# Performance work log

Hardware: AMD Instinct MI355X
Metric: run time of the kernel (lower is better)

The kernel has to match this reference:

```python
import jax, jax.numpy as jnp
import numpy as np
from jax import lax

TOP_K = 2
NHEAD = 8

def _ln(x, g, b, eps=1e-5):
    m = x.mean(-1, keepdims=True)
    v = x.var(-1, keepdims=True)
    return (x - m) / jnp.sqrt(v + eps) * g + b


def setup_inputs() -> dict:
    B, S, N = 32, 512, 32
    DT, D, E, HE, MO, LTX, LTCN, K = 64, 128, 16, 256, 128, 2, 4, 3
    keys = iter(jax.random.split(jax.random.key(0), 96))
    def rn(shape, s=0.05):
        return (jax.random.normal(next(keys), shape, jnp.float32) * s)
    inp = {}
    inp['x_features_globally_std'] = jax.random.normal(next(keys), (B, S, N), jnp.float32)
    counts = jax.random.randint(next(keys), (B,), 8, N + 1)
    inp['sensor_mask'] = (jnp.arange(N)[None, :] < counts[:, None]).astype(jnp.float32)
    inp['proj_w'] = rn((1, DT)); inp['proj_b'] = jnp.zeros(DT)
    inp['tcn_w1'] = rn((LTCN, DT, DT, K)); inp['tcn_b1'] = jnp.zeros((LTCN, DT))
    inp['tcn_w2'] = rn((LTCN, DT, DT, K)); inp['tcn_b2'] = jnp.zeros((LTCN, DT))
    inp['tcn_ln_g'] = jnp.ones(DT); inp['tcn_ln_b'] = jnp.zeros(DT)
    inp['pool_w'] = rn((DT, D)); inp['pool_b'] = jnp.zeros(D)
    inp['pos_inter'] = rn((1, N, D), 0.02)
    inp['tx_ln1_g'] = jnp.ones((LTX, D)); inp['tx_ln1_b'] = jnp.zeros((LTX, D))
    inp['tx_qkv_w'] = rn((LTX, D, 3 * D)); inp['tx_qkv_b'] = jnp.zeros((LTX, 3 * D))
    inp['tx_out_w'] = rn((LTX, D, D)); inp['tx_out_b'] = jnp.zeros((LTX, D))
    inp['tx_ln2_g'] = jnp.ones((LTX, D)); inp['tx_ln2_b'] = jnp.zeros((LTX, D))
    inp['tx_ff1_w'] = rn((LTX, D, 2 * D)); inp['tx_ff1_b'] = jnp.zeros((LTX, 2 * D))
    inp['tx_ff2_w'] = rn((LTX, 2 * D, D)); inp['tx_ff2_b'] = jnp.zeros((LTX, D))
    inp['tx_fln_g'] = jnp.ones(D); inp['tx_fln_b'] = jnp.zeros(D)
    inp['exp_w1'] = rn((E, D, HE)); inp['exp_b1'] = jnp.zeros((E, HE))
    inp['exp_w2'] = rn((E, HE, MO)); inp['exp_b2'] = jnp.zeros((E, MO))
    inp['gate_f_w'] = rn((2 * D, E)); inp['gate_f_b'] = jnp.zeros(E)
    inp['gate_fail_w'] = rn((2 * D, E)); inp['gate_fail_b'] = jnp.zeros(E)
    inp['gate_rca_w'] = rn((D, E)); inp['gate_rca_b'] = jnp.zeros(E)
    inp['pred_w'] = rn((DT + D + MO, 3)); inp['pred_b'] = jnp.zeros(3)
    inp['fail_w'] = rn((MO, 3)); inp['fail_b'] = jnp.zeros(3)
    inp['rca_w'] = rn((DT + D + MO, 1)); inp['rca_b'] = jnp.zeros(1)
    return inp


def reference(x_features_globally_std, sensor_mask, proj_w, proj_b, tcn_w1, tcn_b1, tcn_w2, tcn_b2,
              tcn_ln_g, tcn_ln_b, pool_w, pool_b, pos_inter, tx_ln1_g, tx_ln1_b, tx_qkv_w, tx_qkv_b,
              tx_out_w, tx_out_b, tx_ln2_g, tx_ln2_b, tx_ff1_w, tx_ff1_b, tx_ff2_w, tx_ff2_b,
              tx_fln_g, tx_fln_b, exp_w1, exp_b1, exp_w2, exp_b2, gate_f_w, gate_f_b,
              gate_fail_w, gate_fail_b, gate_rca_w, gate_rca_b, pred_w, pred_b, fail_w, fail_b, rca_w, rca_b):
    x = x_features_globally_std
    B, S, N = x.shape
    DT = proj_w.shape[1]; D = pool_w.shape[1]; E = gate_f_b.shape[0]
    K = tcn_w1.shape[-1]
    # per-sensor encoder: [B,S,N] -> [B*N, S, 1]
    x_enc = x.transpose(0, 2, 1).reshape(B * N, S, 1)
    h = x_enc @ proj_w + proj_b  # [BN,S,DT]
    # sinusoidal positional encoding
    pos = jnp.arange(S, dtype=jnp.float32)[:, None]
    div = jnp.exp(jnp.arange(0, DT, 2, dtype=jnp.float32) * (-np.log(10000.0) / DT))
    pe = jnp.zeros((S, DT), jnp.float32).at[:, 0::2].set(jnp.sin(pos * div)).at[:, 1::2].set(jnp.cos(pos * div))
    h = h + pe
    h = h.transpose(0, 2, 1)  # [BN, DT, S]
    for i in range(tcn_w1.shape[0]):
        dil = 2 ** i
        pad = (K - 1) * dil  # causal left pad == torch pad-both + trim right
        def conv(z, w, b):
            return lax.conv_general_dilated(z, w, (1,), [(pad, 0)], rhs_dilation=(dil,),
                                            dimension_numbers=('NCH', 'OIH', 'NCH')) + b[None, :, None]
        o = jax.nn.relu(conv(h, tcn_w1[i], tcn_b1[i]))
        o = jax.nn.relu(conv(o, tcn_w2[i], tcn_b2[i]))
        h = jax.nn.relu(o + h)  # proj_dim == tcn_out_dim -> no downsample
    h = _ln(h.transpose(0, 2, 1), tcn_ln_g, tcn_ln_b)  # [BN,S,DT]
    st = h.reshape(B, N, S, DT) * sensor_mask[:, :, None, None]
    pooled = st.mean(2)  # [B,N,DT]
    z = pooled @ pool_w + pool_b  # [B,N,D]
    z = z + pos_inter[0, :N]
    pad_mask = sensor_mask == 0  # [B,N] True = padded key
    hd = D // NHEAD
    for l in range(tx_qkv_w.shape[0]):
        y = _ln(z, tx_ln1_g[l], tx_ln1_b[l])
        qkv = y @ tx_qkv_w[l] + tx_qkv_b[l]
        q, k_, v = jnp.split(qkv, 3, -1)
        q = q.reshape(B, N, NHEAD, hd).transpose(0, 2, 1, 3)
        k_ = k_.reshape(B, N, NHEAD, hd).transpose(0, 2, 1, 3)
        v = v.reshape(B, N, NHEAD, hd).transpose(0, 2, 1, 3)
        scores = jnp.einsum('bhqd,bhkd->bhqk', q, k_) / jnp.sqrt(jnp.float32(hd))
        scores = jnp.where(pad_mask[:, None, None, :], -1e9, scores)
        attn = jax.nn.softmax(scores, -1)
        o = jnp.einsum('bhqk,bhkd->bhqd', attn, v).transpose(0, 2, 1, 3).reshape(B, N, D)
        z = z + o @ tx_out_w[l] + tx_out_b[l]
        y = _ln(z, tx_ln2_g[l], tx_ln2_b[l])
        z = z + jax.nn.relu(y @ tx_ff1_w[l] + tx_ff1_b[l]) @ tx_ff2_w[l] + tx_ff2_b[l]
    z = _ln(z, tx_fln_g, tx_fln_b)
    ctx = z * sensor_mask[..., None]  # [B,N,D]
    cnt = jnp.clip(sensor_mask.sum(1, keepdims=True), 1.0, None)
    mean_ctx = ctx.sum(1) / cnt
    var_ctx = (ctx ** 2).sum(1) / cnt - mean_ctx ** 2
    router_in = jnp.concatenate([mean_ctx, jnp.sqrt(jnp.clip(var_ctx, 1e-6, None))], -1)  # [B,2D]

    def moe(xin, gin, gw, gb):
        logits = gin @ gw + gb  # [n,E]
        tv, ti = lax.top_k(logits, TOP_K)
        w = jax.nn.softmax(tv, -1)
        h1 = jax.nn.relu(jnp.einsum('nd,edh->neh', xin, exp_w1) + exp_b1)
        allo = jnp.einsum('neh,eho->neo', h1, exp_w2) + exp_b2  # dense all-expert, per torch code
        sel = jnp.take_along_axis(allo, ti[:, :, None], 1)
        y = (sel * w[:, :, None]).sum(1)
        probs = jax.nn.softmax(logits, -1)
        frac = jnp.zeros((E,), probs.dtype).at[ti.reshape(-1)].add(1.0) / (xin.shape[0] * TOP_K)
        loss = E * (probs.mean(0) * frac).sum()
        return y, loss

    moe_f, aux_f = moe(mean_ctx, router_in, gate_f_w, gate_f_b)
    moe_fail, _ = moe(mean_ctx, router_in, gate_fail_w, gate_fail_b)
    tok = ctx.reshape(B * N, D)
    moe_rca, _ = moe(tok, tok, gate_rca_w, gate_rca_b)
    moe_rca = (moe_rca * sensor_mask.reshape(-1, 1)).reshape(B, N, -1)  # zero invalid tokens
    st_last = st[:, :, -1, :]  # [B,N,DT]
    moe_f_exp = jnp.broadcast_to(moe_f[:, None, :], (B, N, moe_f.shape[-1]))
    pred_in = jnp.concatenate([st_last, ctx, moe_f_exp], -1)
    pred = pred_in @ pred_w + pred_b  # [B,N,pred_horizons]
    fail = moe_fail @ fail_w + fail_b  # [B,fail_horizons]
    rca_in = jnp.concatenate([st_last, ctx, moe_rca], -1)
    rca = (rca_in @ rca_w + rca_b)[..., 0]  # [B,N]
    return pred, fail, rca, aux_f
```

## Files before the change

kernel.cpp:

```cpp
#include <hip/hip_runtime.h>
#include <hip/hip_bf16.h>
#include <math.h>

typedef short short8v __attribute__((ext_vector_type(8)));
typedef float f32x4 __attribute__((ext_vector_type(4)));
typedef unsigned short ushort4v __attribute__((ext_vector_type(4)));

__device__ inline float waveReduceSum(float v){
  #pragma unroll
  for (int off = 32; off > 0; off >>= 1) v += __shfl_xor(v, off, 64);
  return v;
}

__device__ inline unsigned short f2bf(float x){
  unsigned int u = __builtin_bit_cast(unsigned int, x);
  unsigned int r = (u + 0x7FFFu + ((u >> 16) & 1u)) >> 16;
  return (unsigned short)r;
}
__device__ inline float bf2f(unsigned short u){
  unsigned int w = ((unsigned int)u) << 16;
  return __builtin_bit_cast(float, w);
}

__global__ void init_kernel(const float* __restrict__ w1, const float* __restrict__ w2,
                            unsigned short* __restrict__ wf, float* __restrict__ petab){
  int idx = blockIdx.x * 256 + threadIdx.x;
  if (idx < 98304){
    int conv = idx / 12288;
    int r = idx % 12288;
    int tap = r >> 12;
    int kk  = (r >> 11) & 1;
    int ct  = (r >> 9) & 3;
    int lane= (r >> 3) & 63;
    int j   = r & 7;
    int layer = conv >> 1;
    const float* src = (conv & 1) ? w2 : w1;
    int co = (ct << 4) + (lane & 15);
    int ci = (kk << 5) + ((lane >> 4) << 3) + j;
    float v = src[((layer * 64 + co) * 64 + ci) * 3 + tap];
    unsigned short hi = f2bf(v);
    unsigned short lo = f2bf(v - bf2f(hi));
    size_t base = (size_t)conv * 24576 + (size_t)(((tap * 2 + kk) * 4 + ct) * 2) * 512 + lane * 8 + j;
    wf[base] = hi;
    wf[base + 512] = lo;
  } else if (idx < 131072){
    int p = idx - 98304;
    int t = p >> 6, c = p & 63;
    float ang = (float)t * expf(-0.14391156831f * (float)(c & ~1));
    petab[p] = (c & 1) ? cosf(ang) : sinf(ang);
  }
}

template<int DIL, int MODE>
__global__ __launch_bounds__(512, 2) void tcn_fused_kernel(
    const unsigned short* __restrict__ hin, unsigned short* __restrict__ hout,
    const unsigned short* __restrict__ wfrag,
    const float* __restrict__ b1, const float* __restrict__ b2, int convbase,
    const float* __restrict__ x, const float* __restrict__ petab,
    const float* __restrict__ pw, const float* __restrict__ pb,
    const float* __restrict__ lng, const float* __restrict__ lnb,
    const float* __restrict__ maskg,
    float* __restrict__ pooled4, float* __restrict__ stlast, int halfbase){
  constexpr int O_OFF = 40960;
  __shared__ __align__(16) char lds[79872];
  const int tid = threadIdx.x;
  const int lane = tid & 63, wid = tid >> 6;
  const int cp = wid & 1, tsub = wid >> 1;
  const int bnl = blockIdx.x >> 2, cidx = blockIdx.x & 3;
  const int t0 = cidx << 7;
  const int bn = halfbase + bnl;

  if (MODE == 1){
    const int bb = bn >> 5, nn = bn & 31;
    for (int i = 0; i < 3; ++i){
      int idx = tid + i * 512;
      if (idx < 1280){
        int row = idx >> 3, cg = idx & 7;
        int t = t0 - 32 + row;
        short8v vh = {0,0,0,0,0,0,0,0}, vl = {0,0,0,0,0,0,0,0};
        if (t >= 0){
          float xv = x[((size_t)bb << 14) + t * 32 + nn];
          const float* per = petab + t * 64 + cg * 8;
          #pragma unroll
          for (int j = 0; j < 8; ++j){
            int c = cg * 8 + j;
            float val = fmaf(xv, pw[c], pb[c]) + per[j];
            unsigned short h = f2bf(val);
            vh[j] = (short)h;
            vl[j] = (short)f2bf(val - bf2f(h));
          }
        }
        int sw = (row & 7) << 4;
        int base = (row << 8) + (cg << 4);
        *(short8v*)(lds + (base ^ sw)) = vh;
        *(short8v*)(lds + ((base + 128) ^ sw)) = vl;
      }
    }
  } else {
    #pragma unroll
    for (int i = 0; i < 5; ++i){
      int idx = tid + i * 512;
      int row = idx >> 4, c16 = idx & 15;
      int t = t0 - 32 + row;
      short8v v = {0,0,0,0,0,0,0,0};
      if (t >= 0) v = *(const short8v*)(hin + (size_t)(bnl * 512 + t) * 128 + c16 * 8);
      int base = (row << 8) + (c16 << 4);
      *(short8v*)(lds + (base ^ ((row & 7) << 4))) = v;
    }
  }

  short8v A1[3][2][2][2];
  #pragma unroll
  for (int tap = 0; tap < 3; ++tap)
    #pragma unroll
    for (int kk = 0; kk < 2; ++kk)
      #pragma unroll
      for (int cc = 0; cc < 2; ++cc)
        #pragma unroll
        for (int pl = 0; pl < 2; ++pl){
          int ct = 2 * cp + cc;
          A1[tap][kk][cc][pl] = *(const short8v*)(wfrag + (size_t)convbase * 24576 +
              (size_t)((((tap * 2 + kk) * 4 + ct) * 2 + pl)) * 512 + lane * 8);
        }
  __syncthreads();

  for (int S = 0; S < 3; ++S){
    int rbase = (S << 6) + (tsub << 4);
    if (rbase >= 144) continue;
    f32x4 acc0 = {0.f,0.f,0.f,0.f}, acc1 = {0.f,0.f,0.f,0.f};
    int orow = rbase + (lane & 15);
    #pragma unroll
    for (int tap = 0; tap < 3; ++tap){
      int hr = orow + 16 - (2 - tap) * DIL;
      int sw = (hr & 7) << 4;
      #pragma unroll
      for (int kk = 0; kk < 2; ++kk){
        int base = (hr << 8) + (kk << 6) + ((lane >> 4) << 4);
        short8v Bhi = *(const short8v*)(lds + (base ^ sw));
        short8v Blo = *(const short8v*)(lds + ((base + 128) ^ sw));
        acc0 = __builtin_amdgcn_mfma_f32_16x16x32_bf16(A1[tap][kk][0][0], Bhi, acc0, 0, 0, 0);
        acc0 = __builtin_amdgcn_mfma_f32_16x16x32_bf16(A1[tap][kk][0][0], Blo, acc0, 0, 0, 0);
        acc0 = __builtin_amdgcn_mfma_f32_16x16x32_bf16(A1[tap][kk][0][1], Bhi, acc0, 0, 0, 0);
        acc1 = __builtin_amdgcn_mfma_f32_16x16x32_bf16(A1[tap][kk][1][0], Bhi, acc1, 0, 0, 0);
        acc1 = __builtin_amdgcn_mfma_f32_16x16x32_bf16(A1[tap][kk][1][0], Blo, acc1, 0, 0, 0);
        acc1 = __builtin_amdgcn_mfma_f32_16x16x32_bf16(A1[tap][kk][1][1], Bhi, acc1, 0, 0, 0);
      }
    }
    int t_o = t0 - 16 + orow;
    int swO = (orow & 7) << 4;
    #pragma unroll
    for (int cc = 0; cc < 2; ++cc){
      int ct = 2 * cp + cc;
      int cobase = (ct << 4) + ((lane >> 4) << 2);
      ushort4v hi4, lo4;
      #pragma unroll
      for (int r = 0; r < 4; ++r){
        float a = (cc == 0) ? acc0[r] : acc1[r];
        float v = fmaxf(a + b1[cobase + r], 0.f);
        if (t_o < 0) v = 0.f;
        unsigned short h = f2bf(v);
        hi4[r] = h;
        lo4[r] = f2bf(v - bf2f(h));
      }
      int ob = O_OFF + (orow << 8) + (cobase << 1);
      *(ushort4v*)(lds + (ob ^ swO)) = hi4;
      *(ushort4v*)(lds + ((ob + 128) ^ swO)) = lo4;
    }
  }

  short8v A2[3][2][2][2];
  #pragma unroll
  for (int tap = 0; tap < 3; ++tap)
    #pragma unroll
    for (int kk = 0; kk < 2; ++kk)
      #pragma unroll
      for (int cc = 0; cc < 2; ++cc)
        #pragma unroll
        for (int pl = 0; pl < 2; ++pl){
          int ct = 2 * cp + cc;
          A2[tap][kk][cc][pl] = *(const short8v*)(wfrag + (size_t)(convbase + 1) * 24576 +
              (size_t)((((tap * 2 + kk) * 4 + ct) * 2 + pl)) * 512 + lane * 8);
        }
  __syncthreads();

  for (int S = 0; S < 2; ++S){
    f32x4 acc0 = {0.f,0.f,0.f,0.f}, acc1 = {0.f,0.f,0.f,0.f};
    int tt = (S << 6) + (tsub << 4) + (lane & 15);
    #pragma unroll
    for (int tap = 0; tap < 3; ++tap){
      int rb = tt + 16 - (2 - tap) * DIL;
      int sw = (rb & 7) << 4;
      #pragma unroll
      for (int kk = 0; kk < 2; ++kk){
        int base = O_OFF + (rb << 8) + (kk << 6) + ((lane >> 4) << 4);
        short8v Bhi = *(const short8v*)(lds + (base ^ sw));
        short8v Blo = *(const short8v*)(lds + ((base + 128) ^ sw));
        acc0 = __builtin_amdgcn_mfma_f32_16x16x32_bf16(A2[tap][kk][0][0], Bhi, acc0, 0, 0, 0);
        acc0 = __builtin_amdgcn_mfma_f32_16x16x32_bf16(A2[tap][kk][0][0], Blo, acc0, 0, 0, 0);
        acc0 = __builtin_amdgcn_mfma_f32_16x16x32_bf16(A2[tap][kk][0][1], Bhi, acc0, 0, 0, 0);
        acc1 = __builtin_amdgcn_mfma_f32_16x16x32_bf16(A2[tap][kk][1][0], Bhi, acc1, 0, 0, 0);
        acc1 = __builtin_amdgcn_mfma_f32_16x16x32_bf16(A2[tap][kk][1][0], Blo, acc1, 0, 0, 0);
        acc1 = __builtin_amdgcn_mfma_f32_16x16x32_bf16(A2[tap][kk][1][1], Bhi, acc1, 0, 0, 0);
      }
    }
    int rowH = tt + 32;
    int swH = (rowH & 7) << 4;
    if (MODE != 2){
      int t = t0 + tt;
      #pragma unroll
      for (int cc = 0; cc < 2; ++cc){
        int ct = 2 * cp + cc;
        int cobase = (ct << 4) + ((lane >> 4) << 2);
        int rb2 = (rowH << 8) + (cobase << 1);
        ushort4v rhi = *(const ushort4v*)(lds + (rb2 ^ swH));
        ushort4v rlo = *(const ushort4v*)(lds + ((rb2 + 128) ^ swH));
        ushort4v hi4, lo4;
        #pragma unroll
        for (int r = 0; r < 4; ++r){
          float a = (cc == 0) ? acc0[r] : acc1[r];
          float v = fmaxf(a + b2[cobase + r], 0.f);
          v = fmaxf(v + bf2f(rhi[r]) + bf2f(rlo[r]), 0.f);
          unsigned short h = f2bf(v);
          hi4[r] = h;
          lo4[r] = f2bf(v - bf2f(h));
        }
        unsigned short* orow_p = hout + (size_t)(bnl * 512 + t) * 128;
        *(ushort4v*)(orow_p + cobase)      = hi4;
        *(ushort4v*)(orow_p + 64 + cobase) = lo4;
      }
    } else {
      __syncthreads();
      int swO = (tt & 7) << 4;
      #pragma unroll
      for (int cc = 0; cc < 2; ++cc){
        int ct = 2 * cp + cc;
        int cobase = (ct << 4) + ((lane >> 4) << 2);
        int rb2 = (rowH << 8) + (cobase << 1);
        ushort4v rhi = *(const ushort4v*)(lds + (rb2 ^ swH));
        ushort4v rlo = *(const ushort4v*)(lds + ((rb2 + 128) ^ swH));
        f32x4 vv;
        #pragma unroll
        for (int r = 0; r < 4; ++r){
          float a = (cc == 0) ? acc0[r] : acc1[r];
          float v = fmaxf(a + b2[cobase + r], 0.f);
          vv[r] = fmaxf(v + bf2f(rhi[r]) + bf2f(rlo[r]), 0.f);
        }
        *(f32x4*)(lds + ((O_OFF + (tt << 8) + (cobase << 2)) ^ swO)) = vv;
      }
    }
  }

  if (MODE == 2){
    __syncthreads();
    {
      const int row = tid >> 2, q = tid & 3;
      const int sw = (row & 7) << 4;
      float v[16];
      #pragma unroll
      for (int u = 0; u < 4; ++u){
        f32x4 t4 = *(const f32x4*)(lds + ((O_OFF + (row << 8) + q * 64 + u * 16) ^ sw));
        v[u*4+0] = t4[0]; v[u*4+1] = t4[1]; v[u*4+2] = t4[2]; v[u*4+3] = t4[3];
      }
      float s = 0.f, s2 = 0.f;
      #pragma unroll
      for (int j = 0; j < 16; ++j){ s += v[j]; s2 += v[j]*v[j]; }
      s  += __shfl_xor(s, 1, 64);  s  += __shfl_xor(s, 2, 64);
      s2 += __shfl_xor(s2, 1, 64); s2 += __shfl_xor(s2, 2, 64);
      float mean = s * (1.f/64.f);
      float var = s2 * (1.f/64.f) - mean * mean;
      float rstd = rsqrtf(var + 1e-5f);
      #pragma unroll
      for (int j = 0; j < 16; ++j){
        int c = q * 16 + j;
        v[j] = (v[j] - mean) * rstd * lng[c] + lnb[c];
      }
      #pragma unroll
      for (int u = 0; u < 4; ++u){
        f32x4 t4 = { v[u*4+0], v[u*4+1], v[u*4+2], v[u*4+3] };
        *(f32x4*)(lds + ((O_OFF + (row << 8) + q * 64 + u * 16) ^ sw)) = t4;
      }
    }
    __syncthreads();
    {
      int s8 = tid >> 6, c = tid & 63;
      float acc = 0.f;
      #pragma unroll
      for (int r = 0; r < 16; ++r){
        int row = s8 * 16 + r;
        acc += *(const float*)(lds + ((O_OFF + (row << 8) + c * 4) ^ ((row & 7) << 4)));
      }
      *(float*)(lds + 77824 + (s8 * 64 + c) * 4) = acc;
    }
    __syncthreads();
    if (tid < 64){
      float tot = 0.f;
      #pragma unroll
      for (int ss = 0; ss < 8; ++ss) tot += *(const float*)(lds + 77824 + (ss * 64 + tid) * 4);
      pooled4[((size_t)(cidx << 10) + bn) * 64 + tid] = tot;
    }
    if (cidx == 3 && tid >= 64 && tid < 128){
      int c = tid - 64;
      float lv = *(const float*)(lds + ((O_OFF + (127 << 8) + c * 4) ^ ((127 & 7) << 4)));
      stlast[(size_t)bn * 64 + c] = lv * maskg[bn];
    }
  }
}

__global__ __launch_bounds__(1024) void batch_kernel(
    const float* __restrict__ pooled4, const float* __restrict__ maskg,
    const float* __restrict__ pool_w, const float* __restrict__ pool_b,
    const float* __restrict__ pos,
    const float* __restrict__ ln1g, const float* __restrict__ ln1b,
    const float* __restrict__ qkvw, const float* __restrict__ qkvb_g,
    const float* __restrict__ outw, const float* __restrict__ outb,
    const float* __restrict__ ln2g, const float* __restrict__ ln2b,
    const float* __restrict__ ff1w, const float* __restrict__ ff1b,
    const float* __restrict__ ff2w, const float* __restrict__ ff2b,
    const float* __restrict__ flng, const float* __restrict__ flnb,
    const float* __restrict__ ew1, const float* __restrict__ eb1,
    const float* __restrict__ ew2, const float* __restrict__ eb2,
    const float* __restrict__ gfw, const float* __restrict__ gfb,
    const float* __restrict__ gfailw, const float* __restrict__ gfailb,
    const float* __restrict__ failw, const float* __restrict__ failb,
    float* __restrict__ ctxg, float* __restrict__ moefg,
    float* __restrict__ logitsfg, int* __restrict__ tifg,
    float* __restrict__ outg){
  __shared__ float zf[32][128];
  __shared__ float ybuf[32][128];
  __shared__ float qkvb[32][385];
  __shared__ float sc[8][33][33];
  __shared__ float ps[32][64];
  __shared__ float msk[32];
  __shared__ float rin[256];
  __shared__ float meanc[128];
  __shared__ float h1all[4][256];
  __shared__ float oall[4][128];
  __shared__ float lf[16], lfail[16];
  __shared__ int   tisel[4];
  __shared__ float twsel[4];
  __shared__ float moefail[128];
  __shared__ float cntS;

  const int b = blockIdx.x;
  const int tid = threadIdx.x;
  const int lane = tid & 63;

  if (tid < 32) msk[tid] = maskg[b * 32 + tid];
  #pragma unroll
  for (int i = 0; i < 2; ++i){
    int item = tid + 1024 * i;
    int n = item >> 6, c = item & 63;
    float s = 0.f;
    #pragma unroll
    for (int q = 0; q < 4; ++q) s += pooled4[(size_t)q * 65536 + (b * 32 + n) * 64 + c];
    ps[n][c] = s * (1.f / 512.f) * maskg[b * 32 + n];
  }
  __syncthreads();

  {
    int jb = tid & 63, nb = tid >> 6;
    float acc[2][2];
    #pragma unroll
    for (int nn = 0; nn < 2; ++nn)
      #pragma unroll
      for (int jj = 0; jj < 2; ++jj){
        int d = jb * 2 + jj, n = nb * 2 + nn;
        acc[nn][jj] = pool_b[d] + pos[n * 128 + d];
      }
    for (int k = 0; k < 64; ++k){
      float w0 = pool_w[k * 128 + jb * 2], w1 = pool_w[k * 128 + jb * 2 + 1];
      #pragma unroll
      for (int nn = 0; nn < 2; ++nn){
        float y = ps[nb * 2 + nn][k];
        acc[nn][0] += y * w0; acc[nn][1] += y * w1;
      }
    }
    #pragma unroll
    for (int nn = 0; nn < 2; ++nn){
      zf[nb * 2 + nn][jb * 2]     = acc[nn][0];
      zf[nb * 2 + nn][jb * 2 + 1] = acc[nn][1];
    }
  }
  __syncthreads();

  for (int l = 0; l < 2; ++l){
    const float* Wq = qkvw + (size_t)l * 49152;
    const float* bq = qkvb_g + l * 384;
    const float* Wo = outw + (size_t)l * 16384;
    const float* bo = outb + l * 128;
    const float* W1 = ff1w + (size_t)l * 32768;
    const float* bf1 = ff1b + l * 256;
    const float* W2 = ff2w + (size_t)l * 32768;
    const float* bf2 = ff2b + l * 128;
    const float* g1 = ln1g + l * 128; const float* bb1 = ln1b + l * 128;
    const float* g2 = ln2g + l * 128; const float* bb2 = ln2b + l * 128;

    #pragma unroll
    for (int rr = 0; rr < 2; ++rr){
      int row = (tid >> 6) * 2 + rr;
      float x0 = zf[row][lane], x1 = zf[row][lane + 64];
      float mean = waveReduceSum(x0 + x1) * (1.f / 128.f);
      float d0 = x0 - mean, d1 = x1 - mean;
      float var = waveReduceSum(d0 * d0 + d1 * d1) * (1.f / 128.f);
      float rstd = rsqrtf(var + 1e-5f);
      ybuf[row][lane]      = d0 * rstd * g1[lane] + bb1[lane];
      ybuf[row][lane + 64] = d1 * rstd * g1[lane + 64] + bb1[lane + 64];
    }
    __syncthreads();

    {
      int jb = tid & 127, nb = tid >> 7;
      float acc[4][3];
      #pragma unroll
      for (int nn = 0; nn < 4; ++nn)
        #pragma unroll
        for (int jj = 0; jj < 3; ++jj) acc[nn][jj] = 0.f;
      for (int k = 0; k < 128; ++k){
        float w0 = Wq[k * 384 + jb * 3], w1 = Wq[k * 384 + jb * 3 + 1], w2v = Wq[k * 384 + jb * 3 + 2];
        #pragma unroll
        for (int nn = 0; nn < 4; ++nn){
          float y = ybuf[nb * 4 + nn][k];
          acc[nn][0] += y * w0; acc[nn][1] += y * w1; acc[nn][2] += y * w2v;
        }
      }
      #pragma unroll
      for (int nn = 0; nn < 4; ++nn)
        #pragma unroll
        for (int jj = 0; jj < 3; ++jj)
          qkvb[nb * 4 + nn][jb * 3 + jj] = acc[nn][jj] + bq[jb * 3 + jj];
    }
    __syncthreads();

    #pragma unroll
    for (int i = 0; i < 8; ++i){
      int item = tid + 1024 * i;
      int hh = item >> 10, qi = (item >> 5) & 31, ki = item & 31;
      float a = 0.f;
      #pragma unroll
      for (int d = 0; d < 16; ++d) a += qkvb[qi][hh * 16 + d] * qkvb[ki][128 + hh * 16 + d];
      a *= 0.25f;
      if (msk[ki] == 0.f) a = -1e9f;
      sc[hh][qi][ki] = a;
    }
    __syncthreads();
    {
      int row = tid >> 2, q4 = tid & 3;
      int hh = row >> 5, qi = row & 31;
      float v[8];
      float m = -1e30f;
      #pragma unroll
      for (int j = 0; j < 8; ++j){ v[j] = sc[hh][qi][q4 * 8 + j]; m = fmaxf(m, v[j]); }
      m = fmaxf(m, __shfl_xor(m, 1, 64));
      m = fmaxf(m, __shfl_xor(m, 2, 64));
      float s = 0.f;
      #pragma unroll
      for (int j = 0; j < 8; ++j){ v[j] = expf(v[j] - m); s += v[j]; }
      s += __shfl_xor(s, 1, 64);
      s += __shfl_xor(s, 2, 64);
      float inv = 1.f / s;
      #pragma unroll
      for (int j = 0; j < 8; ++j) sc[hh][qi][q4 * 8 + j] = v[j] * inv;
    }
    __syncthreads();
    #pragma unroll
    for (int i = 0; i < 4; ++i){
      int item = tid + 1024 * i;
      int n = item >> 7, dd = item & 127, hh = dd >> 4;
      float o = 0.f;
      #pragma unroll
      for (int ki = 0; ki < 32; ++ki) o += sc[hh][n][ki] * qkvb[ki][256 + dd];
      ybuf[n][dd] = o;
    }
    __syncthreads();

    {
      int jb = tid & 63, nb = tid >> 6;
      float acc[2][2];
      #pragma unroll
      for (int nn = 0; nn < 2; ++nn){ acc[nn][0] = 0.f; acc[nn][1] = 0.f; }
      for (int k = 0; k < 128; ++k){
        float w0 = Wo[k * 128 + jb * 2], w1 = Wo[k * 128 + jb * 2 + 1];
        #pragma unroll
        for (int nn = 0; nn < 2; ++nn){
          float y = ybuf[nb * 2 + nn][k];
          acc[nn][0] += y * w0; acc[nn][1] += y * w1;
        }
      }
      #pragma unroll
      for (int nn = 0; nn < 2; ++nn){
        zf[nb * 2 + nn][jb * 2]     += acc[nn][0] + bo[jb * 2];
        zf[nb * 2 + nn][jb * 2 + 1] += acc[nn][1] + bo[jb * 2 + 1];
      }
    }
    __syncthreads();

    #pragma unroll
    for (int rr = 0; rr < 2; ++rr){
      int row = (tid >> 6) * 2 + rr;
      float x0 = zf[row][lane], x1 = zf[row][lane + 64];
      float mean = waveReduceSum(x0 + x1) * (1.f / 128.f);
      float d0 = x0 - mean, d1 = x1 - mean;
      float var = waveReduceSum(d0 * d0 + d1 * d1) * (1.f / 128.f);
      float rstd = rsqrtf(var + 1e-5f);
      ybuf[row][lane]      = d0 * rstd * g2[lane] + bb2[lane];
      ybuf[row][lane + 64] = d1 * rstd * g2[lane + 64] + bb2[lane + 64];
    }
    __syncthreads();

    {
      int jb = tid & 127, nb = tid >> 7;
      float acc[4][2];
      #pragma unroll
      for (int nn = 0; nn < 4; ++nn){ acc[nn][0] = 0.f; acc[nn][1] = 0.f; }
      for (int k = 0; k < 128; ++k){
        float w0 = W1[k * 256 + jb * 2], w1 = W1[k * 256 + jb * 2 + 1];
        #pragma unroll
        for (int nn = 0; nn < 4; ++nn){
          float y = ybuf[nb * 4 + nn][k];
          acc[nn][0] += y * w0; acc[nn][1] += y * w1;
        }
      }
      #pragma unroll
      for (int nn = 0; nn < 4; ++nn){
        qkvb[nb * 4 + nn][jb * 2]     = fmaxf(acc[nn][0] + bf1[jb * 2], 0.f);
        qkvb[nb * 4 + nn][jb * 2 + 1] = fmaxf(acc[nn][1] + bf1[jb * 2 + 1], 0.f);
      }
    }
    __syncthreads();

    {
      int jb = tid & 63, nb = tid >> 6;
      float acc[2][2];
      #pragma unroll
      for (int nn = 0; nn < 2; ++nn){ acc[nn][0] = 0.f; acc[nn][1] = 0.f; }
      for (int k = 0; k < 256; ++k){
        float w0 = W2[k * 128 + jb * 2], w1 = W2[k * 128 + jb * 2 + 1];
        #pragma unroll
        for (int nn = 0; nn < 2; ++nn){
          float y = qkvb[nb * 2 + nn][k];
          acc[nn][0] += y * w0; acc[nn][1] += y * w1;
        }
      }
      #pragma unroll
      for (int nn = 0; nn < 2; ++nn){
        zf[nb * 2 + nn][jb * 2]     += acc[nn][0] + bf2[jb * 2];
        zf[nb * 2 + nn][jb * 2 + 1] += acc[nn][1] + bf2[jb * 2 + 1];
      }
    }
    __syncthreads();
  }

  #pragma unroll
  for (int rr = 0; rr < 2; ++rr){
    int row = (tid >> 6) * 2 + rr;
    float x0 = zf[row][lane], x1 = zf[row][lane + 64];
    float mean = waveReduceSum(x0 + x1) * (1.f / 128.f);
    float d0 = x0 - mean, d1 = x1 - mean;
    float var = waveReduceSum(d0 * d0 + d1 * d1) * (1.f / 128.f);
    float rstd = rsqrtf(var + 1e-5f);
    float mk = msk[row];
    ybuf[row][lane]      = (d0 * rstd * flng[lane] + flnb[lane]) * mk;
    ybuf[row][lane + 64] = (d1 * rstd * flng[lane + 64] + flnb[lane + 64]) * mk;
  }
  if (tid == 0){
    float c = 0.f;
    for (int n = 0; n < 32; ++n) c += maskg[b * 32 + n];
    cntS = fmaxf(c, 1.f);
  }
  __syncthreads();
  #pragma unroll
  for (int i = 0; i < 4; ++i){
    int item = tid + 1024 * i;
    int n = item >> 7, d = item & 127;
    ctxg[(size_t)(b * 32 + n) * 128 + d] = ybuf[n][d];
  }
  if (tid < 128){
    float s = 0.f, s2 = 0.f;
    for (int n = 0; n < 32; ++n){ float v = ybuf[n][tid]; s += v; s2 += v * v; }
    float mean = s / cntS;
    float var = s2 / cntS - mean * mean;
    meanc[tid] = mean;
    rin[tid] = mean;
    rin[128 + tid] = sqrtf(fmaxf(var, 1e-6f));
  }
  __syncthreads();
  {
    int g = tid >> 9;
    int e = (tid >> 5) & 15, kk = tid & 31;
    const float* gw = g ? gfailw : gfw;
    float a = 0.f;
    #pragma unroll
    for (int j = 0; j < 8; ++j){
      int k = kk * 8 + j;
      a += rin[k] * gw[k * 16 + e];
    }
    a += __shfl_xor(a, 1, 64);  a += __shfl_xor(a, 2, 64);
    a += __shfl_xor(a, 4, 64);  a += __shfl_xor(a, 8, 64);
    a += __shfl_xor(a, 16, 64);
    if (kk == 0){
      if (g == 0){
        float r = a + gfb[e];
        lf[e] = r;
        logitsfg[b * 16 + e] = r;
      } else {
        lfail[e] = a + gfailb[e];
      }
    }
  }
  __syncthreads();
  if (tid < 2){
    const float* lg = (tid == 0) ? lf : lfail;
    int i0 = 0; float v0 = lg[0];
    for (int e = 1; e < 16; ++e) if (lg[e] > v0){ v0 = lg[e]; i0 = e; }
    int i1 = -1; float v1 = -1e30f;
    for (int e = 0; e < 16; ++e) if (e != i0 && lg[e] > v1){ v1 = lg[e]; i1 = e; }
    float e1 = expf(v1 - v0);
    float den = 1.f / (1.f + e1);
    tisel[tid * 2] = i0; tisel[tid * 2 + 1] = i1;
    twsel[tid * 2] = den; twsel[tid * 2 + 1] = e1 * den;
    if (tid == 0){ tifg[b * 2] = i0; tifg[b * 2 + 1] = i1; }
  }
  __syncthreads();
  {
    int sel = tid >> 8, h = tid & 255;
    int e = tisel[sel];
    float a = eb1[e * 256 + h];
    for (int k = 0; k < 128; ++k) a += meanc[k] * ew1[(size_t)(e * 128 + k) * 256 + h];
    h1all[sel][h] = fmaxf(a, 0.f);
  }
  __syncthreads();
  if (tid < 512){
    int sel = tid >> 7, d = tid & 127;
    int e = tisel[sel];
    float o = eb2[e * 128 + d];
    for (int k = 0; k < 256; ++k) o += h1all[sel][k] * ew2[(size_t)(e * 256 + k) * 128 + d];
    oall[sel][d] = twsel[sel] * o;
  }
  __syncthreads();
  if (tid < 128){
    moefg[b * 128 + tid] = oall[0][tid] + oall[1][tid];
    moefail[tid] = oall[2][tid] + oall[3][tid];
  }
  __syncthreads();
  if (tid < 3){
    float a = failb[tid];
    for (int k = 0; k < 128; ++k) a += moefail[k] * failw[k * 3 + tid];
    outg[3072 + b * 3 + tid] = a;
  }
}

__global__ void gate_kernel(const float* __restrict__ gin, const float* __restrict__ gw,
                            const float* __restrict__ gb, int ntok, int K,
                            int* __restrict__ ti, float* __restrict__ tw,
                            float* __restrict__ logits_out){
  int tok = blockIdx.x * 64 + threadIdx.x;
  if (tok >= ntok) return;
  float acc[16];
  #pragma unroll
  for (int e = 0; e < 16; ++e) acc[e] = gb[e];
  const float* gr = gin + (size_t)tok * K;
  for (int k = 0; k < K; ++k){
    float gv = gr[k];
    #pragma unroll
    for (int e = 0; e < 16; ++e) acc[e] = fmaf(gv, gw[k*16 + e], acc[e]);
  }
  if (logits_out){
    #pragma unroll
    for (int e = 0; e < 16; ++e) logits_out[tok*16 + e] = acc[e];
  }
  int i0 = 0; float v0 = acc[0];
  #pragma unroll
  for (int e = 1; e < 16; ++e) if (acc[e] > v0){ v0 = acc[e]; i0 = e; }
  int i1 = -1; float v1 = -1e30f;
  #pragma unroll
  for (int e = 0; e < 16; ++e) if (e != i0 && acc[e] > v1){ v1 = acc[e]; i1 = e; }
  float e1 = expf(v1 - v0);
  float den = 1.f / (1.f + e1);
  ti[tok*2] = i0; ti[tok*2+1] = i1;
  tw[tok*2] = den; tw[tok*2+1] = e1 * den;
}

__global__ void moe_expert_kernel(const float* __restrict__ xin, const int* __restrict__ ti,
                                  const float* __restrict__ tw,
                                  const float* __restrict__ w1, const float* __restrict__ b1,
                                  const float* __restrict__ w2, const float* __restrict__ b2,
                                  const float* __restrict__ mask, float* __restrict__ yout){
  int tok = blockIdx.x;
  int tid = threadIdx.x;
  __shared__ float xs[128];
  __shared__ float h1[256];
  if (tid < 128) xs[tid] = xin[(size_t)tok*128 + tid];
  __syncthreads();
  float accv = 0.f;
  for (int kkk = 0; kkk < 2; ++kkk){
    int e = ti[tok*2 + kkk];
    float wv = tw[tok*2 + kkk];
    float a = b1[e*256 + tid];
    for (int k = 0; k < 128; ++k) a = fmaf(xs[k], w1[(size_t)(e*128 + k)*256 + tid], a);
    __syncthreads();
    h1[tid] = fmaxf(a, 0.f);
    __syncthreads();
    if (tid < 128){
      float o = b2[e*128 + tid];
      for (int k = 0; k < 256; ++k) o = fmaf(h1[k], w2[(size_t)(e*256 + k)*128 + tid], o);
      accv += wv * o;
    }
  }
  if (tid < 128){
    if (mask) accv *= mask[tok];
    yout[(size_t)tok*128 + tid] = accv;
  }
}

__global__ void aux_kernel(const float* __restrict__ logits, const int* __restrict__ ti,
                           float* __restrict__ out_scalar){
  if (threadIdx.x != 0 || blockIdx.x != 0) return;
  float pm[16];
  for (int e = 0; e < 16; ++e) pm[e] = 0.f;
  for (int i = 0; i < 32; ++i){
    const float* row = logits + i*16;
    float m = -1e30f;
    for (int e = 0; e < 16; ++e) m = fmaxf(m, row[e]);
    float s = 0.f;
    float ex[16];
    for (int e = 0; e < 16; ++e){ ex[e] = expf(row[e] - m); s += ex[e]; }
    for (int e = 0; e < 16; ++e) pm[e] += ex[e] / s;
  }
  float cnt[16];
  for (int e = 0; e < 16; ++e) cnt[e] = 0.f;
  for (int i = 0; i < 64; ++i) cnt[ti[i]] += 1.f;
  float loss = 0.f;
  for (int e = 0; e < 16; ++e) loss += (pm[e] / 32.f) * (cnt[e] / 64.f);
  out_scalar[0] = 16.f * loss;
}

__global__ void heads_kernel(const float* __restrict__ st_last, const float* __restrict__ ctx,
                             const float* __restrict__ moe_f, const float* __restrict__ moe_rca,
                             const float* __restrict__ pred_w, const float* __restrict__ pred_b,
                             const float* __restrict__ rca_w, const float* __restrict__ rca_b,
                             float* __restrict__ out){
  int bn = blockIdx.x * 256 + threadIdx.x;
  if (bn >= 1024) return;
  int b = bn >> 5;
  float p0 = pred_b[0], p1 = pred_b[1], p2 = pred_b[2];
  float r = rca_b[0];
  for (int i = 0; i < 64; ++i){
    float v = st_last[(size_t)bn*64 + i];
    p0 = fmaf(v, pred_w[i*3+0], p0); p1 = fmaf(v, pred_w[i*3+1], p1); p2 = fmaf(v, pred_w[i*3+2], p2);
    r = fmaf(v, rca_w[i], r);
  }
  for (int i = 0; i < 128; ++i){
    float v = ctx[(size_t)bn*128 + i];
    int ii = 64 + i;
    p0 = fmaf(v, pred_w[ii*3+0], p0); p1 = fmaf(v, pred_w[ii*3+1], p1); p2 = fmaf(v, pred_w[ii*3+2], p2);
    r = fmaf(v, rca_w[ii], r);
  }
  for (int i = 0; i < 128; ++i){
    int ii = 192 + i;
    float vp = moe_f[(size_t)b*128 + i];
    p0 = fmaf(vp, pred_w[ii*3+0], p0); p1 = fmaf(vp, pred_w[ii*3+1], p1); p2 = fmaf(vp, pred_w[ii*3+2], p2);
    float vr = moe_rca[(size_t)bn*128 + i];
    r = fmaf(vr, rca_w[ii], r);
  }
  out[bn*3+0] = p0; out[bn*3+1] = p1; out[bn*3+2] = p2;
  out[3168 + bn] = r;
}

extern "C" void kernel_launch(void* const* d_in, const int* in_sizes, int n_in,
                              void* d_out, int out_size, void* d_ws, size_t ws_size,
                              hipStream_t stream){
  const float* x        = (const float*)d_in[0];
  const float* mask     = (const float*)d_in[1];
  const float* proj_w   = (const float*)d_in[2];
  const float* proj_b   = (const float*)d_in[3];
  const float* tcn_w1   = (const float*)d_in[4];
  const float* tcn_b1   = (const float*)d_in[5];
  const float* tcn_w2   = (const float*)d_in[6];
  const float* tcn_b2   = (const float*)d_in[7];
  const float* tcn_ln_g = (const float*)d_in[8];
  const float* tcn_ln_b = (const float*)d_in[9];
  const float* pool_w   = (const float*)d_in[10];
  const float* pool_b   = (const float*)d_in[11];
  const float* pos_inter= (const float*)d_in[12];
  const float* tx_ln1_g = (const float*)d_in[13];
  const float* tx_ln1_b = (const float*)d_in[14];
  const float* tx_qkv_w = (const float*)d_in[15];
  const float* tx_qkv_b = (const float*)d_in[16];
  const float* tx_out_w = (const float*)d_in[17];
  const float* tx_out_b = (const float*)d_in[18];
  const float* tx_ln2_g = (const float*)d_in[19];
  const float* tx_ln2_b = (const float*)d_in[20];
  const float* tx_ff1_w = (const float*)d_in[21];
  const float* tx_ff1_b = (const float*)d_in[22];
  const float* tx_ff2_w = (const float*)d_in[23];
  const float* tx_ff2_b = (const float*)d_in[24];
  const float* tx_fln_g = (const float*)d_in[25];
  const float* tx_fln_b = (const float*)d_in[26];
  const float* exp_w1   = (const float*)d_in[27];
  const float* exp_b1   = (const float*)d_in[28];
  const float* exp_w2   = (const float*)d_in[29];
  const float* exp_b2   = (const float*)d_in[30];
  const float* gate_f_w = (const float*)d_in[31];
  const float* gate_f_b = (const float*)d_in[32];
  const float* gate_fail_w = (const float*)d_in[33];
  const float* gate_fail_b = (const float*)d_in[34];
  const float* gate_rca_w  = (const float*)d_in[35];
  const float* gate_rca_b  = (const float*)d_in[36];
  const float* pred_w   = (const float*)d_in[37];
  const float* pred_b   = (const float*)d_in[38];
  const float* fail_w   = (const float*)d_in[39];
  const float* fail_b   = (const float*)d_in[40];
  const float* rca_w    = (const float*)d_in[41];
  const float* rca_b    = (const float*)d_in[42];
  float* out = (float*)d_out;
  float* W = (float*)d_ws;

  const size_t o_pooled4 = 0;
  const size_t o_stlast  = 262144;
  const size_t o_ctx     = 327680;
  const size_t o_moef    = 458752;
  const size_t o_moerca  = 462848;
  const size_t o_logitsf = 593920;
  const size_t o_tif     = 594432;
  const size_t o_twrca   = 594496;
  const size_t o_tirca   = 596544;
  const size_t o_petab   = 598592;
  unsigned short* wfragU = (unsigned short*)(W + 631360);
  unsigned short* hA     = (unsigned short*)((char*)d_ws + 3312640);
  unsigned short* hB     = hA + 33554432;

  init_kernel<<<512, 256, 0, stream>>>(tcn_w1, tcn_w2, wfragU, W + o_petab);

  for (int half = 0; half < 2; ++half){
    int hb = half * 512;
    tcn_fused_kernel<1,1><<<2048, 512, 0, stream>>>(
        nullptr, hB, wfragU, tcn_b1,       tcn_b2,       0,
        x, W + o_petab, proj_w, proj_b,
        nullptr, nullptr, nullptr, nullptr, nullptr, hb);
    tcn_fused_kernel<2,0><<<2048, 512, 0, stream>>>(
        hB, hA, wfragU, tcn_b1 + 64,  tcn_b2 + 64,  2,
        nullptr, nullptr, nullptr, nullptr,
        nullptr, nullptr, nullptr, nullptr, nullptr, hb);
    tcn_fused_kernel<4,0><<<2048, 512, 0, stream>>>(
        hA, hB, wfragU, tcn_b1 + 128, tcn_b2 + 128, 4,
        nullptr, nullptr, nullptr, nullptr,
        nullptr, nullptr, nullptr, nullptr, nullptr, hb);
    tcn_fused_kernel<8,2><<<2048, 512, 0, stream>>>(
        hB, nullptr, wfragU, tcn_b1 + 192, tcn_b2 + 192, 6,
        nullptr, nullptr, nullptr, nullptr,
        tcn_ln_g, tcn_ln_b, mask, W + o_pooled4, W + o_stlast, hb);
  }

  batch_kernel<<<32, 1024, 0, stream>>>(
      W + o_pooled4, mask, pool_w, pool_b, pos_inter,
      tx_ln1_g, tx_ln1_b, tx_qkv_w, tx_qkv_b, tx_out_w, tx_out_b,
      tx_ln2_g, tx_ln2_b, tx_ff1_w, tx_ff1_b, tx_ff2_w, tx_ff2_b,
      tx_fln_g, tx_fln_b,
      exp_w1, exp_b1, exp_w2, exp_b2,
      gate_f_w, gate_f_b, gate_fail_w, gate_fail_b, fail_w, fail_b,
      W + o_ctx, W + o_moef, W + o_logitsf, (int*)(W + o_tif), out);

  gate_kernel<<<16, 64, 0, stream>>>(W + o_ctx, gate_rca_w, gate_rca_b, 1024, 128,
                                     (int*)(W + o_tirca), W + o_twrca, nullptr);
  moe_expert_kernel<<<1024, 256, 0, stream>>>(W + o_ctx, (int*)(W + o_tirca), W + o_twrca,
                                              exp_w1, exp_b1, exp_w2, exp_b2, mask, W + o_moerca);

  aux_kernel<<<1, 64, 0, stream>>>(W + o_logitsf, (int*)(W + o_tif), out + 4192);
  heads_kernel<<<4, 256, 0, stream>>>(W + o_stlast, W + o_ctx, W + o_moef, W + o_moerca,
                                      pred_w, pred_b, rca_w, rca_b, out);
}
```

Baseline: 934.0 us.

## Fuse all TCN layers into one persistent per-sequence kernel keeping activations in LDS

Replaces the eight TCN layer launches, which round-trip hi/lo bf16 activations through global memory, with one kernel per (batch, sensor) sequence. The whole 512-step sequence stays in about 160 KB of LDS, and the kernel walks time chunks backward so the residual update can run in place. LayerNorm, pooling and the last-step output are folded into its epilogue, so the extra pooled4 partial reduction goes away. Launch and global traffic costs drop, but the grid has only 1024 large-LDS blocks with occupancy of one block per CU, many more barriers, and weights reloaded per chunk. Unroll pragmas are also added to many scalar loops elsewhere.

```diff
diff --git a/kernel.cpp b/kernel.cpp
--- a/kernel.cpp
+++ b/kernel.cpp
@@ -51,263 +51,223 @@
   }
 }
 
-template<int DIL, int MODE>
-__global__ __launch_bounds__(512, 2) void tcn_fused_kernel(
-    const unsigned short* __restrict__ hin, unsigned short* __restrict__ hout,
-    const unsigned short* __restrict__ wfrag,
-    const float* __restrict__ b1, const float* __restrict__ b2, int convbase,
-    const float* __restrict__ x, const float* __restrict__ petab,
+__global__ __launch_bounds__(512, 2) void tcn_persist_kernel(
+    const float* __restrict__ x, const unsigned short* __restrict__ wfrag,
+    const float* __restrict__ b1g, const float* __restrict__ b2g,
+    const float* __restrict__ petab,
     const float* __restrict__ pw, const float* __restrict__ pb,
     const float* __restrict__ lng, const float* __restrict__ lnb,
     const float* __restrict__ maskg,
-    float* __restrict__ pooled4, float* __restrict__ stlast, int halfbase){
-  constexpr int O_OFF = 40960;
-  __shared__ __align__(16) char lds[79872];
+    float* __restrict__ pooled, float* __restrict__ stlast){
+  constexpr int O_OFF = 139264;
+  constexpr int P_OFF = 159744;
+  __shared__ __align__(16) char lds[161792];
   const int tid = threadIdx.x;
   const int lane = tid & 63, wid = tid >> 6;
   const int cp = wid & 1, tsub = wid >> 1;
-  const int bnl = blockIdx.x >> 2, cidx = blockIdx.x & 3;
-  const int t0 = cidx << 7;
-  const int bn = halfbase + bnl;
-
-  if (MODE == 1){
-    const int bb = bn >> 5, nn = bn & 31;
-    for (int i = 0; i < 3; ++i){
-      int idx = tid + i * 512;
-      if (idx < 1280){
-        int row = idx >> 3, cg = idx & 7;
-        int t = t0 - 32 + row;
-        short8v vh = {0,0,0,0,0,0,0,0}, vl = {0,0,0,0,0,0,0,0};
-        if (t >= 0){
-          float xv = x[((size_t)bb << 14) + t * 32 + nn];
-          const float* per = petab + t * 64 + cg * 8;
+  const int bn = blockIdx.x;
+  const int bb = bn >> 5, nn = bn & 31;
+
+  for (int i = 0; i < 9; ++i){
+    int idx = tid + i * 512;
+    if (idx < 4352){
+      int row = idx >> 3, cg = idx & 7;
+      int t = row - 32;
+      short8v vh = {0,0,0,0,0,0,0,0}, vl = {0,0,0,0,0,0,0,0};
+      if (t >= 0){
+        float xv = x[((size_t)bb << 14) + (t << 5) + nn];
+        const float* per = petab + t * 64 + cg * 8;
+        #pragma unroll
+        for (int j = 0; j < 8; ++j){
+          int c = cg * 8 + j;
+          float val = fmaf(xv, pw[c], pb[c]) + per[j];
+          unsigned short h = f2bf(val);
+          vh[j] = (short)h;
+          vl[j] = (short)f2bf(val - bf2f(h));
+        }
+      }
+      int sw = (row & 7) << 4;
+      int base = (row << 8) + (cg << 4);
+      *(short8v*)(lds + (base ^ sw)) = vh;
+      *(short8v*)(lds + ((base + 128) ^ sw)) = vl;
+    }
+  }
+
+  const int cobase0 = ((2 * cp) << 4) + ((lane >> 4) << 2);
+  const int cobase1 = ((2 * cp + 1) << 4) + ((lane >> 4) << 2);
+
+  for (int layer = 0; layer < 4; ++layer){
+    const int dil = 1 << layer;
+    const int convbase = layer * 2;
+    f32x4 b1v0 = *(const f32x4*)(b1g + (layer << 6) + cobase0);
+    f32x4 b1v1 = *(const f32x4*)(b1g + (layer << 6) + cobase1);
+    f32x4 b2v0 = *(const f32x4*)(b2g + (layer << 6) + cobase0);
+    f32x4 b2v1 = *(const f32x4*)(b2g + (layer << 6) + cobase1);
+
+    for (int ch = 7; ch >= 0; --ch){
+      const int t0 = ch << 6;
+      __syncthreads();
+
+      short8v A1[3][2][2][2];
+      #pragma unroll
+      for (int tap = 0; tap < 3; ++tap)
+        #pragma unroll
+        for (int kk = 0; kk < 2; ++kk)
           #pragma unroll
-          for (int j = 0; j < 8; ++j){
-            int c = cg * 8 + j;
-            float val = fmaf(xv, pw[c], pb[c]) + per[j];
-            unsigned short h = f2bf(val);
-            vh[j] = (short)h;
-            vl[j] = (short)f2bf(val - bf2f(h));
+          for (int cc = 0; cc < 2; ++cc)
+            #pragma unroll
+            for (int pl = 0; pl < 2; ++pl){
+              int ct = 2 * cp + cc;
+              A1[tap][kk][cc][pl] = *(const short8v*)(wfrag + (size_t)convbase * 24576 +
+                  (size_t)((((tap * 2 + kk) * 4 + ct) * 2 + pl)) * 512 + lane * 8);
+            }
+
+      for (int S = 0; S < 2; ++S){
+        int rbase = (S << 6) + (tsub << 4);
+        if (rbase >= 80) continue;
+        f32x4 acc0 = {0.f,0.f,0.f,0.f}, acc1 = {0.f,0.f,0.f,0.f};
+        int orow = rbase + (lane & 15);
+        int t_o = t0 - 16 + orow;
+        #pragma unroll
+        for (int tap = 0; tap < 3; ++tap){
+          int hr = t_o - (2 - tap) * dil + 32;
+          int sw = (hr & 7) << 4;
+          #pragma unroll
+          for (int kk = 0; kk < 2; ++kk){
+            int base = (hr << 8) + (kk << 6) + ((lane >> 4) << 4);
+            short8v Bhi = *(const short8v*)(lds + (base ^ sw));
+            short8v Blo = *(const short8v*)(lds + ((base + 128) ^ sw));
+            acc0 = __builtin_amdgcn_mfma_f32_16x16x32_bf16(A1[tap][kk][0][0], Bhi, acc0, 0, 0, 0);
+            acc0 = __builtin_amdgcn_mfma_f32_16x16x32_bf16(A1[tap][kk][0][0], Blo, acc0, 0, 0, 0);
+            acc0 = __builtin_amdgcn_mfma_f32_16x16x32_bf16(A1[tap][kk][0][1], Bhi, acc0, 0, 0, 0);
+            acc1 = __builtin_amdgcn_mfma_f32_16x16x32_bf16(A1[tap][kk][1][0], Bhi, acc1, 0, 0, 0);
+            acc1 = __builtin_amdgcn_mfma_f32_16x16x32_bf16(A1[tap][kk][1][0], Blo, acc1, 0, 0, 0);
+            acc1 = __builtin_amdgcn_mfma_f32_16x16x32_bf16(A1[tap][kk][1][1], Bhi, acc1, 0, 0, 0);
           }
         }
-        int sw = (row & 7) << 4;
-        int base = (row << 8) + (cg << 4);
-        *(short8v*)(lds + (base ^ sw)) = vh;
-        *(short8v*)(lds + ((base + 128) ^ sw)) = vl;
-      }
-    }
-  } else {
-    #pragma unroll
-    for (int i = 0; i < 5; ++i){
-      int idx = tid + i * 512;
-      int row = idx >> 4, c16 = idx & 15;
-      int t = t0 - 32 + row;
-      short8v v = {0,0,0,0,0,0,0,0};
-      if (t >= 0) v = *(const short8v*)(hin + (size_t)(bnl * 512 + t) * 128 + c16 * 8);
-      int base = (row << 8) + (c16 << 4);
-      *(short8v*)(lds + (base ^ ((row & 7) << 4))) = v;
-    }
-  }
-
-  short8v A1[3][2][2][2];
-  #pragma unroll
-  for (int tap = 0; tap < 3; ++tap)
-    #pragma unroll
-    for (int kk = 0; kk < 2; ++kk)
-      #pragma unroll
-      for (int cc = 0; cc < 2; ++cc)
-        #pragma unroll
-        for (int pl = 0; pl < 2; ++pl){
-          int ct = 2 * cp + cc;
-          A1[tap][kk][cc][pl] = *(const short8v*)(wfrag + (size_t)convbase * 24576 +
-              (size_t)((((tap * 2 + kk) * 4 + ct) * 2 + pl)) * 512 + lane * 8);
+        int swO = (orow & 7) << 4;
+        #pragma unroll
+        for (int cc = 0; cc < 2; ++cc){
+          int cobase = (cc == 0) ? cobase0 : cobase1;
+          ushort4v hi4, lo4;
+          #pragma unroll
+          for (int r = 0; r < 4; ++r){
+            float a = (cc == 0) ? acc0[r] : acc1[r];
+            float bv = (cc == 0) ? b1v0[r] : b1v1[r];
+            float v = fmaxf(a + bv, 0.f);
+            if (t_o < 0) v = 0.f;
+            unsigned short h = f2bf(v);
+            hi4[r] = h;
+            lo4[r] = f2bf(v - bf2f(h));
+          }
+          int ob = O_OFF + (orow << 8) + (cobase << 1);
+          *(ushort4v*)(lds + (ob ^ swO)) = hi4;
+          *(ushort4v*)(lds + ((ob + 128) ^ swO)) = lo4;
         }
-  __syncthreads();
-
-  for (int S = 0; S < 3; ++S){
-    int rbase = (S << 6) + (tsub << 4);
-    if (rbase >= 144) continue;
-    f32x4 acc0 = {0.f,0.f,0.f,0.f}, acc1 = {0.f,0.f,0.f,0.f};
-    int orow = rbase + (lane & 15);
-    #pragma unroll
-    for (int tap = 0; tap < 3; ++tap){
-      int hr = orow + 16 - (2 - tap) * DIL;
+      }
+
+      short8v A2[3][2][2][2];
+      #pragma unroll
+      for (int tap = 0; tap < 3; ++tap)
+        #pragma unroll
+        for (int kk = 0; kk < 2; ++kk)
+          #pragma unroll
+          for (int cc = 0; cc < 2; ++cc)
+            #pragma unroll
+            for (int pl = 0; pl < 2; ++pl){
+              int ct = 2 * cp + cc;
+              A2[tap][kk][cc][pl] = *(const short8v*)(wfrag + (size_t)(convbase + 1) * 24576 +
+                  (size_t)((((tap * 2 + kk) * 4 + ct) * 2 + pl)) * 512 + lane * 8);
+            }
+      __syncthreads();
+
+      {
+        f32x4 acc0 = {0.f,0.f,0.f,0.f}, acc1 = {0.f,0.f,0.f,0.f};
+        int tt = (tsub << 4) + (lane & 15);
+        #pragma unroll
+        for (int tap = 0; tap < 3; ++tap){
+          int ol = tt + 16 - (2 - tap) * dil;
+          int sw = (ol & 7) << 4;
+          #pragma unroll
+          for (int kk = 0; kk < 2; ++kk){
+            int base = O_OFF + (ol << 8) + (kk << 6) + ((lane >> 4) << 4);
+            short8v Bhi = *(const short8v*)(lds + (base ^ sw));
+            short8v Blo = *(const short8v*)(lds + ((base + 128) ^ sw));
+            acc0 = __builtin_amdgcn_mfma_f32_16x16x32_bf16(A2[tap][kk][0][0], Bhi, acc0, 0, 0, 0);
+            acc0 = __builtin_amdgcn_mfma_f32_16x16x32_bf16(A2[tap][kk][0][0], Blo, acc0, 0, 0, 0);
+            acc0 = __builtin_amdgcn_mfma_f32_16x16x32_bf16(A2[tap][kk][0][1], Bhi, acc0, 0, 0, 0);
+            acc1 = __builtin_amdgcn_mfma_f32_16x16x32_bf16(A2[tap][kk][1][0], Bhi, acc1, 0, 0, 0);
+            acc1 = __builtin_amdgcn_mfma_f32_16x16x32_bf16(A2[tap][kk][1][0], Blo, acc1, 0, 0, 0);
+            acc1 = __builtin_amdgcn_mfma_f32_16x16x32_bf16(A2[tap][kk][1][1], Bhi, acc1, 0, 0, 0);
+          }
+        }
+        int hr = t0 + tt + 32;
+        int swH = (hr & 7) << 4;
+        #pragma unroll
+        for (int cc = 0; cc < 2; ++cc){
+          int cobase = (cc == 0) ? cobase0 : cobase1;
+          int rb = (hr << 8) + (cobase << 1);
+          ushort4v rhi = *(const ushort4v*)(lds + (rb ^ swH));
+          ushort4v rlo = *(const ushort4v*)(lds + ((rb + 128) ^ swH));
+          ushort4v hi4, lo4;
+          #pragma unroll
+          for (int r = 0; r < 4; ++r){
+            float a = (cc == 0) ? acc0[r] : acc1[r];
+            float bv = (cc == 0) ? b2v0[r] : b2v1[r];
+            float v = fmaxf(a + bv, 0.f);
+            v = fmaxf(v + bf2f(rhi[r]) + bf2f(rlo[r]), 0.f);
+            unsigned short h = f2bf(v);
+            hi4[r] = h;
+            lo4[r] = f2bf(v - bf2f(h));
+          }
+          *(ushort4v*)(lds + (rb ^ swH)) = hi4;
+          *(ushort4v*)(lds + ((rb + 128) ^ swH)) = lo4;
+        }
+      }
+    }
+  }
+
+  __syncthreads();
+  {
+    int s8 = tid >> 6, c = tid & 63;
+    float gc = lng[c], bc = lnb[c];
+    float mk = maskg[bn];
+    float acc = 0.f, last = 0.f;
+    for (int r0 = 0; r0 < 64; ++r0){
+      int row = (s8 << 6) + r0;
+      int hr = row + 32;
       int sw = (hr & 7) << 4;
-      #pragma unroll
-      for (int kk = 0; kk < 2; ++kk){
-        int base = (hr << 8) + (kk << 6) + ((lane >> 4) << 4);
-        short8v Bhi = *(const short8v*)(lds + (base ^ sw));
-        short8v Blo = *(const short8v*)(lds + ((base + 128) ^ sw));
-        acc0 = __builtin_amdgcn_mfma_f32_16x16x32_bf16(A1[tap][kk][0][0], Bhi, acc0, 0, 0, 0);
-        acc0 = __builtin_amdgcn_mfma_f32_16x16x32_bf16(A1[tap][kk][0][0], Blo, acc0, 0, 0, 0);
-        acc0 = __builtin_amdgcn_mfma_f32_16x16x32_bf16(A1[tap][kk][0][1], Bhi, acc0, 0, 0, 0);
-        acc1 = __builtin_amdgcn_mfma_f32_16x16x32_bf16(A1[tap][kk][1][0], Bhi, acc1, 0, 0, 0);
-        acc1 = __builtin_amdgcn_mfma_f32_16x16x32_bf16(A1[tap][kk][1][0], Blo, acc1, 0, 0, 0);
-        acc1 = __builtin_amdgcn_mfma_f32_16x16x32_bf16(A1[tap][kk][1][1], Bhi, acc1, 0, 0, 0);
-      }
-    }
-    int t_o = t0 - 16 + orow;
-    int swO = (orow & 7) << 4;
-    #pragma unroll
-    for (int cc = 0; cc < 2; ++cc){
-      int ct = 2 * cp + cc;
-      int cobase = (ct << 4) + ((lane >> 4) << 2);
-      ushort4v hi4, lo4;
-      #pragma unroll
-      for (int r = 0; r < 4; ++r){
-        float a = (cc == 0) ? acc0[r] : acc1[r];
-        float v = fmaxf(a + b1[cobase + r], 0.f);
-        if (t_o < 0) v = 0.f;
-        unsigned short h = f2bf(v);
-        hi4[r] = h;
-        lo4[r] = f2bf(v - bf2f(h));
-      }
-      int ob = O_OFF + (orow << 8) + (cobase << 1);
-      *(ushort4v*)(lds + (ob ^ swO)) = hi4;
-      *(ushort4v*)(lds + ((ob + 128) ^ swO)) = lo4;
-    }
-  }
-
-  short8v A2[3][2][2][2];
-  #pragma unroll
-  for (int tap = 0; tap < 3; ++tap)
-    #pragma unroll
-    for (int kk = 0; kk < 2; ++kk)
-      #pragma unroll
-      for (int cc = 0; cc < 2; ++cc)
-        #pragma unroll
-        for (int pl = 0; pl < 2; ++pl){
-          int ct = 2 * cp + cc;
-          A2[tap][kk][cc][pl] = *(const short8v*)(wfrag + (size_t)(convbase + 1) * 24576 +
-              (size_t)((((tap * 2 + kk) * 4 + ct) * 2 + pl)) * 512 + lane * 8);
-        }
-  __syncthreads();
-
-  for (int S = 0; S < 2; ++S){
-    f32x4 acc0 = {0.f,0.f,0.f,0.f}, acc1 = {0.f,0.f,0.f,0.f};
-    int tt = (S << 6) + (tsub << 4) + (lane & 15);
-    #pragma unroll
-    for (int tap = 0; tap < 3; ++tap){
-      int rb = tt + 16 - (2 - tap) * DIL;
-      int sw = (rb & 7) << 4;
-      #pragma unroll
-      for (int kk = 0; kk < 2; ++kk){
-        int base = O_OFF + (rb << 8) + (kk << 6) + ((lane >> 4) << 4);
-        short8v Bhi = *(const short8v*)(lds + (base ^ sw));
-        short8v Blo = *(const short8v*)(lds + ((base + 128) ^ sw));
-        acc0 = __builtin_amdgcn_mfma_f32_16x16x32_bf16(A2[tap][kk][0][0], Bhi, acc0, 0, 0, 0);
-        acc0 = __builtin_amdgcn_mfma_f32_16x16x32_bf16(A2[tap][kk][0][0], Blo, acc0, 0, 0, 0);
-        acc0 = __builtin_amdgcn_mfma_f32_16x16x32_bf16(A2[tap][kk][0][1], Bhi, acc0, 0, 0, 0);
-        acc1 = __builtin_amdgcn_mfma_f32_16x16x32_bf16(A2[tap][kk][1][0], Bhi, acc1, 0, 0, 0);
-        acc1 = __builtin_amdgcn_mfma_f32_16x16x32_bf16(A2[tap][kk][1][0], Blo, acc1, 0, 0, 0);
-        acc1 = __builtin_amdgcn_mfma_f32_16x16x32_bf16(A2[tap][kk][1][1], Bhi, acc1, 0, 0, 0);
-      }
-    }
-    int rowH = tt + 32;
-    int swH = (rowH & 7) << 4;
-    if (MODE != 2){
-      int t = t0 + tt;
-      #pragma unroll
-      for (int cc = 0; cc < 2; ++cc){
-        int ct = 2 * cp + cc;
-        int cobase = (ct << 4) + ((lane >> 4) << 2);
-        int rb2 = (rowH << 8) + (cobase << 1);
-        ushort4v rhi = *(const ushort4v*)(lds + (rb2 ^ swH));
-        ushort4v rlo = *(const ushort4v*)(lds + ((rb2 + 128) ^ swH));
-        ushort4v hi4, lo4;
-        #pragma unroll
-        for (int r = 0; r < 4; ++r){
-          float a = (cc == 0) ? acc0[r] : acc1[r];
-          float v = fmaxf(a + b2[cobase + r], 0.f);
-          v = fmaxf(v + bf2f(rhi[r]) + bf2f(rlo[r]), 0.f);
-          unsigned short h = f2bf(v);
-          hi4[r] = h;
-          lo4[r] = f2bf(v - bf2f(h));
-        }
-        unsigned short* orow_p = hout + (size_t)(bnl * 512 + t) * 128;
-        *(ushort4v*)(orow_p + cobase)      = hi4;
-        *(ushort4v*)(orow_p + 64 + cobase) = lo4;
-      }
-    } else {
-      __syncthreads();
-      int swO = (tt & 7) << 4;
-      #pragma unroll
-      for (int cc = 0; cc < 2; ++cc){
-        int ct = 2 * cp + cc;
-        int cobase = (ct << 4) + ((lane >> 4) << 2);
-        int rb2 = (rowH << 8) + (cobase << 1);
-        ushort4v rhi = *(const ushort4v*)(lds + (rb2 ^ swH));
-        ushort4v rlo = *(const ushort4v*)(lds + ((rb2 + 128) ^ swH));
-        f32x4 vv;
-        #pragma unroll
-        for (int r = 0; r < 4; ++r){
-          float a = (cc == 0) ? acc0[r] : acc1[r];
-          float v = fmaxf(a + b2[cobase + r], 0.f);
-          vv[r] = fmaxf(v + bf2f(rhi[r]) + bf2f(rlo[r]), 0.f);
-        }
-        *(f32x4*)(lds + ((O_OFF + (tt << 8) + (cobase << 2)) ^ swO)) = vv;
-      }
-    }
-  }
-
-  if (MODE == 2){
-    __syncthreads();
-    {
-      const int row = tid >> 2, q = tid & 3;
-      const int sw = (row & 7) << 4;
-      float v[16];
-      #pragma unroll
-      for (int u = 0; u < 4; ++u){
-        f32x4 t4 = *(const f32x4*)(lds + ((O_OFF + (row << 8) + q * 64 + u * 16) ^ sw));
-        v[u*4+0] = t4[0]; v[u*4+1] = t4[1]; v[u*4+2] = t4[2]; v[u*4+3] = t4[3];
-      }
-      float s = 0.f, s2 = 0.f;
-      #pragma unroll
-      for (int j = 0; j < 16; ++j){ s += v[j]; s2 += v[j]*v[j]; }
-      s  += __shfl_xor(s, 1, 64);  s  += __shfl_xor(s, 2, 64);
-      s2 += __shfl_xor(s2, 1, 64); s2 += __shfl_xor(s2, 2, 64);
-      float mean = s * (1.f/64.f);
-      float var = s2 * (1.f/64.f) - mean * mean;
+      int base = (hr << 8) + (c << 1);
+      float hi = bf2f(*(const unsigned short*)(lds + (base ^ sw)));
+      float lo = bf2f(*(const unsigned short*)(lds + ((base + 128) ^ sw)));
+      float val = hi + lo;
+      float sum = val, sq = val * val;
+      #pragma unroll
+      for (int off = 32; off > 0; off >>= 1){
+        sum += __shfl_xor(sum, off, 64);
+        sq  += __shfl_xor(sq, off, 64);
+      }
+      float mean = sum * (1.f / 64.f);
+      float var = sq * (1.f / 64.f) - mean * mean;
       float rstd = rsqrtf(var + 1e-5f);
-      #pragma unroll
-      for (int j = 0; j < 16; ++j){
-        int c = q * 16 + j;
-        v[j] = (v[j] - mean) * rstd * lng[c] + lnb[c];
-      }
-      #pragma unroll
-      for (int u = 0; u < 4; ++u){
-        f32x4 t4 = { v[u*4+0], v[u*4+1], v[u*4+2], v[u*4+3] };
-        *(f32x4*)(lds + ((O_OFF + (row << 8) + q * 64 + u * 16) ^ sw)) = t4;
-      }
-    }
-    __syncthreads();
-    {
-      int s8 = tid >> 6, c = tid & 63;
-      float acc = 0.f;
-      #pragma unroll
-      for (int r = 0; r < 16; ++r){
-        int row = s8 * 16 + r;
-        acc += *(const float*)(lds + ((O_OFF + (row << 8) + c * 4) ^ ((row & 7) << 4)));
-      }
-      *(float*)(lds + 77824 + (s8 * 64 + c) * 4) = acc;
-    }
+      float o = (val - mean) * rstd * gc + bc;
+      acc += o;
+      if (row == 511) last = o;
+    }
+    *(float*)(lds + P_OFF + ((s8 << 6) + c) * 4) = acc;
+    if (s8 == 7) stlast[(size_t)bn * 64 + c] = last * mk;
     __syncthreads();
     if (tid < 64){
       float tot = 0.f;
       #pragma unroll
-      for (int ss = 0; ss < 8; ++ss) tot += *(const float*)(lds + 77824 + (ss * 64 + tid) * 4);
-      pooled4[((size_t)(cidx << 10) + bn) * 64 + tid] = tot;
-    }
-    if (cidx == 3 && tid >= 64 && tid < 128){
-      int c = tid - 64;
-      float lv = *(const float*)(lds + ((O_OFF + (127 << 8) + c * 4) ^ ((127 & 7) << 4)));
-      stlast[(size_t)bn * 64 + c] = lv * maskg[bn];
+      for (int ss = 0; ss < 8; ++ss) tot += *(const float*)(lds + P_OFF + ((ss << 6) + tid) * 4);
+      pooled[(size_t)bn * 64 + tid] = tot * (1.f / 512.f) * mk;
     }
   }
 }
 
 __global__ __launch_bounds__(1024) void batch_kernel(
-    const float* __restrict__ pooled4, const float* __restrict__ maskg,
+    const float* __restrict__ pooled, const float* __restrict__ maskg,
     const float* __restrict__ pool_w, const float* __restrict__ pool_b,
     const float* __restrict__ pos,
     const float* __restrict__ ln1g, const float* __restrict__ ln1b,
@@ -350,10 +310,7 @@
   for (int i = 0; i < 2; ++i){
     int item = tid + 1024 * i;
     int n = item >> 6, c = item & 63;
-    float s = 0.f;
-    #pragma unroll
-    for (int q = 0; q < 4; ++q) s += pooled4[(size_t)q * 65536 + (b * 32 + n) * 64 + c];
-    ps[n][c] = s * (1.f / 512.f) * maskg[b * 32 + n];
+    ps[n][c] = pooled[(size_t)(b * 32 + n) * 64 + c];
   }
   __syncthreads();
 
@@ -367,6 +324,7 @@
         int d = jb * 2 + jj, n = nb * 2 + nn;
         acc[nn][jj] = pool_b[d] + pos[n * 128 + d];
       }
+    #pragma unroll 8
     for (int k = 0; k < 64; ++k){
       float w0 = pool_w[k * 128 + jb * 2], w1 = pool_w[k * 128 + jb * 2 + 1];
       #pragma unroll
@@ -415,6 +373,7 @@
       for (int nn = 0; nn < 4; ++nn)
         #pragma unroll
         for (int jj = 0; jj < 3; ++jj) acc[nn][jj] = 0.f;
+      #pragma unroll 8
       for (int k = 0; k < 128; ++k){
         float w0 = Wq[k * 384 + jb * 3], w1 = Wq[k * 384 + jb * 3 + 1], w2v = Wq[k * 384 + jb * 3 + 2];
         #pragma unroll
@@ -478,6 +437,7 @@
       float acc[2][2];
       #pragma unroll
       for (int nn = 0; nn < 2; ++nn){ acc[nn][0] = 0.f; acc[nn][1] = 0.f; }
+      #pragma unroll 8
       for (int k = 0; k < 128; ++k){
         float w0 = Wo[k * 128 + jb * 2], w1 = Wo[k * 128 + jb * 2 + 1];
         #pragma unroll
@@ -512,6 +472,7 @@
       float acc[4][2];
       #pragma unroll
       for (int nn = 0; nn < 4; ++nn){ acc[nn][0] = 0.f; acc[nn][1] = 0.f; }
+      #pragma unroll 8
       for (int k = 0; k < 128; ++k){
         float w0 = W1[k * 256 + jb * 2], w1 = W1[k * 256 + jb * 2 + 1];
         #pragma unroll
@@ -533,6 +494,7 @@
       float acc[2][2];
       #pragma unroll
       for (int nn = 0; nn < 2; ++nn){ acc[nn][0] = 0.f; acc[nn][1] = 0.f; }
+      #pragma unroll 8
       for (int k = 0; k < 256; ++k){
         float w0 = W2[k * 128 + jb * 2], w1 = W2[k * 128 + jb * 2 + 1];
         #pragma unroll
@@ -576,6 +538,7 @@
   }
   if (tid < 128){
     float s = 0.f, s2 = 0.f;
+    #pragma unroll 8
     for (int n = 0; n < 32; ++n){ float v = ybuf[n][tid]; s += v; s2 += v * v; }
     float mean = s / cntS;
     float var = s2 / cntS - mean * mean;
@@ -625,6 +588,7 @@
     int sel = tid >> 8, h = tid & 255;
     int e = tisel[sel];
     float a = eb1[e * 256 + h];
+    #pragma unroll 8
     for (int k = 0; k < 128; ++k) a += meanc[k] * ew1[(size_t)(e * 128 + k) * 256 + h];
     h1all[sel][h] = fmaxf(a, 0.f);
   }
@@ -633,6 +597,7 @@
     int sel = tid >> 7, d = tid & 127;
     int e = tisel[sel];
     float o = eb2[e * 128 + d];
+    #pragma unroll 8
     for (int k = 0; k < 256; ++k) o += h1all[sel][k] * ew2[(size_t)(e * 256 + k) * 128 + d];
     oall[sel][d] = twsel[sel] * o;
   }
@@ -659,6 +624,7 @@
   #pragma unroll
   for (int e = 0; e < 16; ++e) acc[e] = gb[e];
   const float* gr = gin + (size_t)tok * K;
+  #pragma unroll 4
   for (int k = 0; k < K; ++k){
     float gv = gr[k];
     #pragma unroll
@@ -696,12 +662,14 @@
     int e = ti[tok*2 + kkk];
     float wv = tw[tok*2 + kkk];
     float a = b1[e*256 + tid];
+    #pragma unroll 8
     for (int k = 0; k < 128; ++k) a = fmaf(xs[k], w1[(size_t)(e*128 + k)*256 + tid], a);
     __syncthreads();
     h1[tid] = fmaxf(a, 0.f);
     __syncthreads();
     if (tid < 128){
       float o = b2[e*128 + tid];
+      #pragma unroll 8
       for (int k = 0; k < 256; ++k) o = fmaf(h1[k], w2[(size_t)(e*256 + k)*128 + tid], o);
       accv += wv * o;
     }
@@ -744,17 +712,20 @@
   int b = bn >> 5;
   float p0 = pred_b[0], p1 = pred_b[1], p2 = pred_b[2];
   float r = rca_b[0];
+  #pragma unroll 4
   for (int i = 0; i < 64; ++i){
     float v = st_last[(size_t)bn*64 + i];
     p0 = fmaf(v, pred_w[i*3+0], p0); p1 = fmaf(v, pred_w[i*3+1], p1); p2 = fmaf(v, pred_w[i*3+2], p2);
     r = fmaf(v, rca_w[i], r);
   }
+  #pragma unroll 4
   for (int i = 0; i < 128; ++i){
     float v = ctx[(size_t)bn*128 + i];
     int ii = 64 + i;
     p0 = fmaf(v, pred_w[ii*3+0], p0); p1 = fmaf(v, pred_w[ii*3+1], p1); p2 = fmaf(v, pred_w[ii*3+2], p2);
     r = fmaf(v, rca_w[ii], r);
   }
+  #pragma unroll 4
   for (int i = 0; i < 128; ++i){
     int ii = 192 + i;
     float vp = moe_f[(size_t)b*128 + i];
@@ -815,44 +786,26 @@
   float* out = (float*)d_out;
   float* W = (float*)d_ws;
 
-  const size_t o_pooled4 = 0;
-  const size_t o_stlast  = 262144;
-  const size_t o_ctx     = 327680;
-  const size_t o_moef    = 458752;
-  const size_t o_moerca  = 462848;
-  const size_t o_logitsf = 593920;
-  const size_t o_tif     = 594432;
-  const size_t o_twrca   = 594496;
-  const size_t o_tirca   = 596544;
-  const size_t o_petab   = 598592;
-  unsigned short* wfragU = (unsigned short*)(W + 631360);
-  unsigned short* hA     = (unsigned short*)((char*)d_ws + 3312640);
-  unsigned short* hB     = hA + 33554432;
+  const size_t o_pooled  = 0;
+  const size_t o_stlast  = 65536;
+  const size_t o_ctx     = 131072;
+  const size_t o_moef    = 262144;
+  const size_t o_moerca  = 266240;
+  const size_t o_logitsf = 397312;
+  const size_t o_tif     = 397824;
+  const size_t o_twrca   = 397888;
+  const size_t o_tirca   = 399936;
+  const size_t o_petab   = 401984;
+  unsigned short* wfragU = (unsigned short*)(W + 434752);
 
   init_kernel<<<512, 256, 0, stream>>>(tcn_w1, tcn_w2, wfragU, W + o_petab);
 
-  for (int half = 0; half < 2; ++half){
-    int hb = half * 512;
-    tcn_fused_kernel<1,1><<<2048, 512, 0, stream>>>(
-        nullptr, hB, wfragU, tcn_b1,       tcn_b2,       0,
-        x, W + o_petab, proj_w, proj_b,
-        nullptr, nullptr, nullptr, nullptr, nullptr, hb);
-    tcn_fused_kernel<2,0><<<2048, 512, 0, stream>>>(
-        hB, hA, wfragU, tcn_b1 + 64,  tcn_b2 + 64,  2,
-        nullptr, nullptr, nullptr, nullptr,
-        nullptr, nullptr, nullptr, nullptr, nullptr, hb);
-    tcn_fused_kernel<4,0><<<2048, 512, 0, stream>>>(
-        hA, hB, wfragU, tcn_b1 + 128, tcn_b2 + 128, 4,
-        nullptr, nullptr, nullptr, nullptr,
-        nullptr, nullptr, nullptr, nullptr, nullptr, hb);
-    tcn_fused_kernel<8,2><<<2048, 512, 0, stream>>>(
-        hB, nullptr, wfragU, tcn_b1 + 192, tcn_b2 + 192, 6,
-        nullptr, nullptr, nullptr, nullptr,
-        tcn_ln_g, tcn_ln_b, mask, W + o_pooled4, W + o_stlast, hb);
-  }
+  tcn_persist_kernel<<<1024, 512, 0, stream>>>(
+      x, wfragU, tcn_b1, tcn_b2, W + o_petab, proj_w, proj_b,
+      tcn_ln_g, tcn_ln_b, mask, W + o_pooled, W + o_stlast);
 
   batch_kernel<<<32, 1024, 0, stream>>>(
-      W + o_pooled4, mask, pool_w, pool_b, pos_inter,
+      W + o_pooled, mask, pool_w, pool_b, pos_inter,
       tx_ln1_g, tx_ln1_b, tx_qkv_w, tx_qkv_b, tx_out_w, tx_out_b,
       tx_ln2_g, tx_ln2_b, tx_ff1_w, tx_ff1_b, tx_ff2_w, tx_ff2_b,
       tx_fln_g, tx_fln_b,
```

Measured after the change: 944.1 us. No clear change (+1.1%).
